# Optimization experiments

Measured on AMD Instinct MI355X. Metric: run time of the kernel, lower is better.

The kernel has to match this reference:

```python
import jax, jax.numpy as jnp
import numpy as np

B, L, DX, DQ = 8, 4096, 128, 128


def setup_inputs() -> dict:
    key = jax.random.key(0)
    ks = jax.random.split(key, 16)
    g = lambda k, shp, fan: jax.random.normal(k, shp, jnp.float32) * (1.0 / np.sqrt(fan))
    return {
        'x': jax.random.normal(ks[0], (B, L, DX), jnp.float32),
        'c': jax.random.normal(ks[1], (B, DQ), jnp.float32),
        # CrossAttention('add') params (all Linear weights stored as (in, out))
        'W1': g(ks[2], (DX, DX), DX),          # w1, bias frozen at 0
        'W2': g(ks[3], (DQ, DX), DQ),          # w2, bias frozen at 0
        'wt_w': g(ks[4], (DX,), DX),           # wt: dx -> 1, bias frozen at 0
        'bsa': jnp.zeros((DX,), jnp.float32),
        # csa pairwise-score params
        'Wsa1': g(ks[5], (DX, DX), DX),        # bias frozen at 0
        'Wsa2': g(ks[6], (DX, DX), DX),        # bias frozen at 0
        'wsat_w': g(ks[7], (DX,), DX),         # wsat: dx -> 1
        'wsat_b': jnp.zeros((), jnp.float32),
        'bsa1': jnp.zeros((DX,), jnp.float32),
        # PositionwiseFeedForward(dx, dx)
        'pfn_w1': g(ks[8], (DX, DX), DX),
        'pfn_b1': jnp.zeros((DX,), jnp.float32),
        'pfn_w2': g(ks[9], (DX, DX), DX),
        'pfn_b2': jnp.zeros((DX,), jnp.float32),
        'ln_g': jnp.ones((DX,), jnp.float32),
        'ln_b': jnp.zeros((DX,), jnp.float32),
    }


def reference(x, c, W1, W2, wt_w, bsa, Wsa1, Wsa2, wsat_w, wsat_b, bsa1,
              pfn_w1, pfn_b1, pfn_w2, pfn_b2, ln_g, ln_b):
    seq_len = x.shape[-2]
    # ---- CrossAttention, mode='add': p = softmax(wt(w1(x) + w2(c) + bsa), dim=-2) ----
    wx = jnp.einsum('bld,de->ble', x, W1)                 # (B, L, dx)
    wq = jnp.einsum('bd,de->be', c, W2)                   # (B, dx)
    logits = jnp.einsum('ble,e->bl', wx + wq[:, None, :] + bsa, wt_w)
    p = jax.nn.softmax(logits, axis=-1)[..., None]        # softmax over L -> (B, L, 1)
    h = x * p                                             # (B, L, dx)
    # ---- pairwise additive scores: wsat(Wsa1(h)_i + Wsa2(h)_j + bsa1) ----
    # wsat is linear, so the (B,L,L,dx) tensor decomposes exactly into rank-1 terms.
    si = jnp.einsum('ble,e->bl', jnp.einsum('bld,de->ble', h, Wsa1), wsat_w)  # (B, L)
    sj = jnp.einsum('ble,e->bl', jnp.einsum('bld,de->ble', h, Wsa2), wsat_w)  # (B, L)
    const = jnp.dot(bsa1, wsat_w) + wsat_b
    scores = jax.nn.sigmoid(si[:, :, None] + sj[:, None, :] + const)          # (B, L, L)
    # mask diagonal with -inf then softmax over last dim (j)
    diag = jnp.eye(seq_len, dtype=bool)
    scores = jnp.where(diag, -jnp.inf, scores)
    A = jax.nn.softmax(scores, axis=-1)                   # (B, L, L)
    # ui = sum_i A[b,i,j] * x[b,j,:]  (faithful to fcsa * x.unsqueeze(1) summed over dim 1)
    ui = x * jnp.sum(A, axis=1)[..., None]                # (B, L, dx)
    # ---- PositionwiseFeedForward with residual + LayerNorm(eps=1e-6); dropout=eval/identity ----
    y = jnp.maximum(jnp.einsum('bld,de->ble', ui, pfn_w1) + pfn_b1, 0.0)
    y = jnp.einsum('ble,ed->bld', y, pfn_w2) + pfn_b2 + ui
    mu = jnp.mean(y, axis=-1, keepdims=True)
    var = jnp.mean(jnp.square(y - mu), axis=-1, keepdims=True)
    return (y - mu) / jnp.sqrt(var + 1e-6) * ln_g + ln_b
```

## Files before the change

### kernel.cpp

```cpp
#include <hip/hip_runtime.h>


#define SEQ 4096
#define NB 8
#define DXC 128
#define SQRTE 1.6487212707001282f
#define Y1S 136

typedef __attribute__((ext_vector_type(8))) short short8;
typedef __attribute__((ext_vector_type(4))) float f32x4;

__device__ __forceinline__ float wave_sum(float v) {
#pragma unroll
  for (int m = 32; m >= 1; m >>= 1) v += __shfl_xor(v, m);
  return v;
}

__device__ __forceinline__ unsigned short f2bf(float f) {
  unsigned int u = __float_as_uint(f);
  unsigned int r = (u + 0x7FFFu + ((u >> 16) & 1u)) >> 16;
  return (unsigned short)r;
}

__device__ __forceinline__ void get_ck(float* ck) {
  ck[0] = 1.0f;
  ck[1] = 0.25f;
  ck[2] = 0.03125f;
  ck[3] = -7.0f / 384.0f;
  ck[4] = -31.0f / 6144.0f;
  ck[5] = 177.0f / 122880.0f;
  ck[6] = 2017.0f / 2949120.0f;
}

__device__ __forceinline__ float binomf(int k, int m) {
  const float B[7][7] = {
      {1, 0, 0, 0, 0, 0, 0},  {1, 1, 0, 0, 0, 0, 0},   {1, 2, 1, 0, 0, 0, 0},
      {1, 3, 3, 1, 0, 0, 0},  {1, 4, 6, 4, 1, 0, 0},   {1, 5, 10, 10, 5, 1, 0},
      {1, 6, 15, 20, 15, 6, 1}};
  return B[k][m];
}

__device__ __forceinline__ float g_exact(float t) {
  float sg = 1.0f / (1.0f + __expf(-t));
  return __expf(sg);
}

__global__ __launch_bounds__(256) void prep_pack(
    const float* __restrict__ W1, const float* __restrict__ W2,
    const float* __restrict__ Wsa1, const float* __restrict__ Wsa2,
    const float* __restrict__ wt_w, const float* __restrict__ wsat_w,
    const float* __restrict__ pw1, const float* __restrict__ pw2,
    float* __restrict__ vecs, unsigned short* __restrict__ Wt1,
    unsigned short* __restrict__ Wt2) {
  if (blockIdx.x < 128) {
    int wave = (blockIdx.x * 256 + threadIdx.x) >> 6;
    int lane = threadIdx.x & 63;
    int m = wave >> 7, d = wave & 127;
    const float* W = (m == 0) ? W1 : (m == 1) ? W2 : (m == 2) ? Wsa1 : Wsa2;
    const float* v = (m < 2) ? wt_w : wsat_w;
    float2 a = ((const float2*)(W + d * DXC))[lane];
    float2 b = ((const float2*)v)[lane];
    float s = wave_sum(a.x * b.x + a.y * b.y);
    if (lane == 0) vecs[m * DXC + d] = s;
  } else {
    int id = (blockIdx.x - 128) * 256 + threadIdx.x;
    int which = id >> 14;
    int k = id & 16383;
    int eo = k >> 7, d = k & 127;
    if (which == 0)
      Wt1[eo * DXC + d] = f2bf(pw1[d * DXC + eo]);
    else
      Wt2[eo * DXC + d] = f2bf(pw2[d * DXC + eo]);
  }
}

__global__ __launch_bounds__(256) void rowdots(
    const float* __restrict__ x, const float* __restrict__ vecs,
    float* __restrict__ t0, float* __restrict__ t1, float* __restrict__ t2) {
  int row = (blockIdx.x * 256 + threadIdx.x) >> 6;
  int lane = threadIdx.x & 63;
  float2 xv = ((const float2*)(x + (size_t)row * DXC))[lane];
  float2 a = ((const float2*)(vecs + 0))[lane];
  float2 b = ((const float2*)(vecs + 256))[lane];
  float2 d = ((const float2*)(vecs + 384))[lane];
  float s0 = wave_sum(xv.x * a.x + xv.y * a.y);
  float s1 = wave_sum(xv.x * b.x + xv.y * b.y);
  float s2 = wave_sum(xv.x * d.x + xv.y * d.y);
  if (lane == 0) { t0[row] = s0; t1[row] = s1; t2[row] = s2; }
}

__global__ __launch_bounds__(1024) void softmax_zq(
    const float* __restrict__ t0, const float* __restrict__ t1,
    const float* __restrict__ t2, const float* __restrict__ c,
    const float* __restrict__ bsa, const float* __restrict__ wt_w,
    const float* __restrict__ bsa1, const float* __restrict__ wsat_w,
    const float* __restrict__ wsat_b, const float* __restrict__ v2,
    float* __restrict__ sj, float* __restrict__ dcol,
    float* __restrict__ Qout) {
  __shared__ float red[16];
  __shared__ float red7[16][7];
  __shared__ float bc[4];
  __shared__ float Sv[8];
  __shared__ float Ps[7];
  int b = blockIdx.x, tid = threadIdx.x;
  if (tid < 64) {
    float2 cv = ((const float2*)(c + b * DXC))[tid];
    float2 vv = ((const float2*)v2)[tid];
    float2 ba = ((const float2*)bsa)[tid];
    float2 wt = ((const float2*)wt_w)[tid];
    float s = wave_sum(cv.x * vv.x + cv.y * vv.y + ba.x * wt.x + ba.y * wt.y);
    float2 b1 = ((const float2*)bsa1)[tid];
    float2 ww = ((const float2*)wsat_w)[tid];
    float t = wave_sum(b1.x * ww.x + b1.y * ww.y);
    if (tid == 0) { bc[2] = s; bc[3] = t + wsat_b[0]; }
  }
  float4 l4 = ((const float4*)(t0 + b * SEQ))[tid];
  __syncthreads();
  float cbv = bc[2], ccst = bc[3];
  l4.x += cbv; l4.y += cbv; l4.z += cbv; l4.w += cbv;
  float m = fmaxf(fmaxf(l4.x, l4.y), fmaxf(l4.z, l4.w));
#pragma unroll
  for (int s = 32; s >= 1; s >>= 1) m = fmaxf(m, __shfl_xor(m, s));
  if ((tid & 63) == 0) red[tid >> 6] = m;
  __syncthreads();
  if (tid < 16) {
    float v = red[tid];
#pragma unroll
    for (int s = 8; s >= 1; s >>= 1) v = fmaxf(v, __shfl_xor(v, s));
    if (tid == 0) bc[0] = v;
  }
  __syncthreads();
  float M = bc[0];
  float e0 = __expf(l4.x - M), e1 = __expf(l4.y - M);
  float e2 = __expf(l4.z - M), e3 = __expf(l4.w - M);
  float s = (e0 + e1) + (e2 + e3);
#pragma unroll
  for (int sh = 32; sh >= 1; sh >>= 1) s += __shfl_xor(s, sh);
  if ((tid & 63) == 0) red[tid >> 6] = s;
  __syncthreads();
  if (tid < 16) {
    float v = red[tid];
#pragma unroll
    for (int sh = 8; sh >= 1; sh >>= 1) v += __shfl_xor(v, sh);
    if (tid == 0) bc[1] = v;
  }
  __syncthreads();
  float inv = 1.0f / bc[1];
  float4 a4 = ((const float4*)(t1 + b * SEQ))[tid];
  float4 bb4 = ((const float4*)(t2 + b * SEQ))[tid];
  float av[4], bv[4];
  av[0] = e0 * inv * a4.x + ccst; av[1] = e1 * inv * a4.y + ccst;
  av[2] = e2 * inv * a4.z + ccst; av[3] = e3 * inv * a4.w + ccst;
  bv[0] = e0 * inv * bb4.x; bv[1] = e1 * inv * bb4.y;
  bv[2] = e2 * inv * bb4.z; bv[3] = e3 * inv * bb4.w;
  ((float4*)(sj + b * SEQ))[tid] = make_float4(bv[0], bv[1], bv[2], bv[3]);
  {
    float sm[6] = {0.f, 0.f, 0.f, 0.f, 0.f, 0.f};
#pragma unroll
    for (int e = 0; e < 4; ++e) {
      float t = bv[e];
#pragma unroll
      for (int n = 0; n < 6; ++n) { sm[n] += t; t *= bv[e]; }
    }
#pragma unroll
    for (int n = 0; n < 6; ++n) sm[n] = wave_sum(sm[n]);
    if ((tid & 63) == 0) {
#pragma unroll
      for (int n = 0; n < 6; ++n) red7[tid >> 6][n] = sm[n];
    }
  }
  __syncthreads();
  if (tid < 6) {
    float acc = 0.f;
#pragma unroll
    for (int w = 0; w < 16; ++w) acc += red7[w][tid];
    Sv[tid + 1] = acc;
  }
  if (tid == 6) Sv[0] = (float)SEQ;
  __syncthreads();
  if (tid < 7) {
    float ck[7];
    get_ck(ck);
    float acc = 0.f;
    for (int n = 0; n <= 6 - tid; ++n)
      acc += ck[tid + n] * binomf(tid + n, tid) * Sv[n];
    Ps[tid] = SQRTE * acc;
  }
  __syncthreads();
  float P0 = Ps[0], P1 = Ps[1], P2 = Ps[2], P3 = Ps[3], P4 = Ps[4],
        P5 = Ps[5], P6 = Ps[6];
  float acc[7] = {0.f, 0.f, 0.f, 0.f, 0.f, 0.f, 0.f};
  float4 dc;
  float* dcp = (float*)&dc;
#pragma unroll
  for (int e = 0; e < 4; ++e) {
    float a = av[e];
    float zf = ((((((P6 * a + P5) * a + P4) * a + P3) * a + P2) * a + P1) * a)
               + P0;
    float d = g_exact(a + bv[e]);
    float iz = 1.0f / (zf - d);
    dcp[e] = d * iz;
    float p = iz;
    acc[0] += p;
#pragma unroll
    for (int n = 1; n < 7; ++n) { p *= a; acc[n] += p; }
  }
  ((float4*)(dcol + b * SEQ))[tid] = dc;
#pragma unroll
  for (int n = 0; n < 7; ++n) acc[n] = wave_sum(acc[n]);
  if ((tid & 63) == 0) {
#pragma unroll
    for (int n = 0; n < 7; ++n) red7[tid >> 6][n] = acc[n];
  }
  __syncthreads();
  if (tid < 7) {
    float t = 0.f;
#pragma unroll
    for (int w = 0; w < 16; ++w) t += red7[w][tid];
    red[tid] = t;
  }
  __syncthreads();
  if (tid < 7) {
    float ck[7];
    get_ck(ck);
    float acc2 = 0.f;
    for (int n = 0; n <= 6 - tid; ++n)
      acc2 += ck[tid + n] * binomf(tid + n, tid) * red[n];
    Qout[b * 8 + tid] = SQRTE * acc2;
  }
}

__global__ __launch_bounds__(256) void ffn_mfma(
    const float* __restrict__ x, const float* __restrict__ sj,
    const float* __restrict__ dcol, const float* __restrict__ Q,
    const unsigned short* __restrict__ Wt1,
    const unsigned short* __restrict__ Wt2,
    const float* __restrict__ b1, const float* __restrict__ b2,
    const float* __restrict__ lng, const float* __restrict__ lnb,
    float* __restrict__ out) {
  __shared__ float cs[64];
  __shared__ __align__(16) unsigned short y1[64 * Y1S];
  int tid = threadIdx.x;
  int base = blockIdx.x * 64;
  int b = blockIdx.x >> 6;
  if (tid < 64) {
    int row = base + tid;
    float bb = sj[row];
    float q0 = Q[b * 8 + 0], q1 = Q[b * 8 + 1], q2 = Q[b * 8 + 2];
    float q3 = Q[b * 8 + 3], q4 = Q[b * 8 + 4], q5 = Q[b * 8 + 5];
    float q6 = Q[b * 8 + 6];
    cs[tid] = ((((((q6 * bb + q5) * bb + q4) * bb + q3) * bb + q2) * bb + q1)
              * bb + q0) - dcol[row];
  }
  __syncthreads();
  int lane = tid & 63, wave = tid >> 6;
  int n16 = lane & 15, quad = lane >> 4;
  int m0 = wave * 16;
  int rowA = base + m0 + n16;
  float csA = cs[m0 + n16];
  const float4* xr = (const float4*)(x + (size_t)rowA * DXC);
  short8 afr[4];
#pragma unroll
  for (int cc = 0; cc < 4; ++cc) {
    float4 p0 = xr[cc * 8 + quad * 2];
    float4 p1 = xr[cc * 8 + quad * 2 + 1];
    short8 af;
    af[0] = (short)f2bf(p0.x * csA); af[1] = (short)f2bf(p0.y * csA);
    af[2] = (short)f2bf(p0.z * csA); af[3] = (short)f2bf(p0.w * csA);
    af[4] = (short)f2bf(p1.x * csA); af[5] = (short)f2bf(p1.y * csA);
    af[6] = (short)f2bf(p1.z * csA); af[7] = (short)f2bf(p1.w * csA);
    afr[cc] = af;
  }
#pragma unroll
  for (int nt = 0; nt < 8; ++nt) {
    const unsigned short* wrow = Wt1 + (nt * 16 + n16) * DXC;
    f32x4 a = {0.f, 0.f, 0.f, 0.f};
#pragma unroll
    for (int cc = 0; cc < 4; ++cc) {
      short8 bf = *(const short8*)(wrow + cc * 32 + quad * 8);
      a = __builtin_amdgcn_mfma_f32_16x16x32_bf16(afr[cc], bf, a, 0, 0, 0);
    }
    float b1v = b1[nt * 16 + n16];
#pragma unroll
    for (int r = 0; r < 4; ++r) {
      float yv = fmaxf(a[r] + b1v, 0.f);
      y1[(m0 + quad * 4 + r) * Y1S + nt * 16 + n16] = f2bf(yv);
    }
  }
  __syncthreads();
  const unsigned short* yrow = &y1[(m0 + n16) * Y1S];
  short8 afr2[4];
#pragma unroll
  for (int cc = 0; cc < 4; ++cc)
    afr2[cc] = *(const short8*)(yrow + cc * 32 + quad * 8);
  f32x4 acc2[8];
#pragma unroll
  for (int nt = 0; nt < 8; ++nt) {
    const unsigned short* wrow = Wt2 + (nt * 16 + n16) * DXC;
    f32x4 a = {0.f, 0.f, 0.f, 0.f};
#pragma unroll
    for (int cc = 0; cc < 4; ++cc) {
      short8 bf = *(const short8*)(wrow + cc * 32 + quad * 8);
      a = __builtin_amdgcn_mfma_f32_16x16x32_bf16(afr2[cc], bf, a, 0, 0, 0);
    }
    acc2[nt] = a;
  }
  float b2v[8], lgv[8], lbv[8];
#pragma unroll
  for (int nt = 0; nt < 8; ++nt) {
    int col = nt * 16 + n16;
    b2v[nt] = b2[col]; lgv[nt] = lng[col]; lbv[nt] = lnb[col];
  }
#pragma unroll
  for (int r = 0; r < 4; ++r) {
    int rl = m0 + quad * 4 + r;
    int row = base + rl;
    float csr = cs[rl];
    const float* xrow = x + (size_t)row * DXC;
    float z[8];
    float s = 0.f, sq = 0.f;
#pragma unroll
    for (int nt = 0; nt < 8; ++nt) {
      int col = nt * 16 + n16;
      float zz = acc2[nt][r] + b2v[nt] + xrow[col] * csr;
      z[nt] = zz; s += zz; sq += zz * zz;
    }
#pragma unroll
    for (int mm = 8; mm >= 1; mm >>= 1) {
      s += __shfl_xor(s, mm);
      sq += __shfl_xor(sq, mm);
    }
    float mu = s * 0.0078125f;
    float var = sq * 0.0078125f - mu * mu;
    float rstd = 1.0f / sqrtf(var + 1e-6f);
    float* orow = out + (size_t)row * DXC;
#pragma unroll
    for (int nt = 0; nt < 8; ++nt) {
      int col = nt * 16 + n16;
      orow[col] = (z[nt] - mu) * rstd * lgv[nt] + lbv[nt];
    }
  }
}

extern "C" void kernel_launch(void* const* d_in, const int* in_sizes, int n_in,
                              void* d_out, int out_size, void* d_ws, size_t ws_size,
                              hipStream_t stream) {
  const float* x = (const float*)d_in[0];
  const float* cc = (const float*)d_in[1];
  const float* W1 = (const float*)d_in[2];
  const float* W2 = (const float*)d_in[3];
  const float* wt_w = (const float*)d_in[4];
  const float* bsa = (const float*)d_in[5];
  const float* Wsa1 = (const float*)d_in[6];
  const float* Wsa2 = (const float*)d_in[7];
  const float* wsat_w = (const float*)d_in[8];
  const float* wsat_b = (const float*)d_in[9];
  const float* bsa1 = (const float*)d_in[10];
  const float* pw1 = (const float*)d_in[11];
  const float* pb1 = (const float*)d_in[12];
  const float* pw2 = (const float*)d_in[13];
  const float* pb2 = (const float*)d_in[14];
  const float* lng = (const float*)d_in[15];
  const float* lnb = (const float*)d_in[16];
  float* out = (float*)d_out;
  float* ws = (float*)d_ws;

  const int NR = NB * SEQ;
  float* vecs = ws;
  float* Q = ws + 512;
  float* t0 = ws + 1024;
  float* t1 = t0 + NR;
  float* t2 = t1 + NR;
  float* sj = t2 + NR;
  float* dcol = sj + NR;
  unsigned short* Wt1 = (unsigned short*)(ws + 164864);
  unsigned short* Wt2 = (unsigned short*)(ws + 164864 + 8192);

  prep_pack<<<256, 256, 0, stream>>>(W1, W2, Wsa1, Wsa2, wt_w, wsat_w, pw1,
                                     pw2, vecs, Wt1, Wt2);
  rowdots<<<NR / 4, 256, 0, stream>>>(x, vecs, t0, t1, t2);
  softmax_zq<<<NB, 1024, 0, stream>>>(t0, t1, t2, cc, bsa, wt_w, bsa1, wsat_w,
                                      wsat_b, vecs + 128, sj, dcol, Q);
  ffn_mfma<<<NR / 64, 256, 0, stream>>>(x, sj, dcol, Q, Wt1, Wt2, pb1, pb2,
                                        lng, lnb, out);
}
```

Measured before the change: 137.4 us.

## Fuse weight prep, row dots and softmax into one per-batch front kernel

Merges prep_pack, rowdots and softmax_zq into a single kernel with one 1024-thread block per batch. Each block computes the weight-vector projections into shared memory, streams its batch's 4096 rows of x to compute the three row dots into shared memory, then runs the softmax and moment reductions. It also drops the softmax max-subtraction and the c/bsa logit offset, since a constant shift cancels in the softmax. This removes two launches and the global round trips for t0/t1/t2, but the 16 MB read of x now runs on only 8 workgroups, which risks being far slower than the wide rowdots grid.

```diff
diff --git a/kernel.cpp b/kernel.cpp
--- a/kernel.cpp
+++ b/kernel.cpp
@@ -13,6 +13,12 @@
 __device__ __forceinline__ float wave_sum(float v) {
 #pragma unroll
   for (int m = 32; m >= 1; m >>= 1) v += __shfl_xor(v, m);
+  return v;
+}
+
+__device__ __forceinline__ float qwave_sum(float v) {
+#pragma unroll
+  for (int m = 8; m >= 1; m >>= 1) v += __shfl_xor(v, m);
   return v;
 }
 
@@ -45,179 +51,173 @@
   return __expf(sg);
 }
 
-__global__ __launch_bounds__(256) void prep_pack(
-    const float* __restrict__ W1, const float* __restrict__ W2,
+__global__ __launch_bounds__(1024) void fused_front(
+    const float* __restrict__ x, const float* __restrict__ W1,
     const float* __restrict__ Wsa1, const float* __restrict__ Wsa2,
     const float* __restrict__ wt_w, const float* __restrict__ wsat_w,
+    const float* __restrict__ wsat_b, const float* __restrict__ bsa1,
     const float* __restrict__ pw1, const float* __restrict__ pw2,
-    float* __restrict__ vecs, unsigned short* __restrict__ Wt1,
-    unsigned short* __restrict__ Wt2) {
-  if (blockIdx.x < 128) {
-    int wave = (blockIdx.x * 256 + threadIdx.x) >> 6;
-    int lane = threadIdx.x & 63;
-    int m = wave >> 7, d = wave & 127;
-    const float* W = (m == 0) ? W1 : (m == 1) ? W2 : (m == 2) ? Wsa1 : Wsa2;
-    const float* v = (m < 2) ? wt_w : wsat_w;
-    float2 a = ((const float2*)(W + d * DXC))[lane];
-    float2 b = ((const float2*)v)[lane];
-    float s = wave_sum(a.x * b.x + a.y * b.y);
-    if (lane == 0) vecs[m * DXC + d] = s;
-  } else {
-    int id = (blockIdx.x - 128) * 256 + threadIdx.x;
-    int which = id >> 14;
-    int k = id & 16383;
-    int eo = k >> 7, d = k & 127;
-    if (which == 0)
-      Wt1[eo * DXC + d] = f2bf(pw1[d * DXC + eo]);
-    else
-      Wt2[eo * DXC + d] = f2bf(pw2[d * DXC + eo]);
-  }
-}
-
-__global__ __launch_bounds__(256) void rowdots(
-    const float* __restrict__ x, const float* __restrict__ vecs,
-    float* __restrict__ t0, float* __restrict__ t1, float* __restrict__ t2) {
-  int row = (blockIdx.x * 256 + threadIdx.x) >> 6;
-  int lane = threadIdx.x & 63;
-  float2 xv = ((const float2*)(x + (size_t)row * DXC))[lane];
-  float2 a = ((const float2*)(vecs + 0))[lane];
-  float2 b = ((const float2*)(vecs + 256))[lane];
-  float2 d = ((const float2*)(vecs + 384))[lane];
-  float s0 = wave_sum(xv.x * a.x + xv.y * a.y);
-  float s1 = wave_sum(xv.x * b.x + xv.y * b.y);
-  float s2 = wave_sum(xv.x * d.x + xv.y * d.y);
-  if (lane == 0) { t0[row] = s0; t1[row] = s1; t2[row] = s2; }
-}
-
-__global__ __launch_bounds__(1024) void softmax_zq(
-    const float* __restrict__ t0, const float* __restrict__ t1,
-    const float* __restrict__ t2, const float* __restrict__ c,
-    const float* __restrict__ bsa, const float* __restrict__ wt_w,
-    const float* __restrict__ bsa1, const float* __restrict__ wsat_w,
-    const float* __restrict__ wsat_b, const float* __restrict__ v2,
+    unsigned short* __restrict__ Wt1, unsigned short* __restrict__ Wt2,
     float* __restrict__ sj, float* __restrict__ dcol,
     float* __restrict__ Qout) {
-  __shared__ float red[16];
-  __shared__ float red7[16][7];
-  __shared__ float bc[4];
-  __shared__ float Sv[8];
-  __shared__ float Ps[7];
+  __shared__ float vs[3 * DXC];
+  __shared__ __align__(16) float t0s[SEQ];
+  __shared__ __align__(16) float t1s[SEQ];
+  __shared__ __align__(16) float t2s[SEQ];
+  __shared__ float red[16][8];
+  __shared__ float bcast[8];
+  __shared__ float Ps[8];
+  __shared__ float ccst_s;
+
   int b = blockIdx.x, tid = threadIdx.x;
-  if (tid < 64) {
-    float2 cv = ((const float2*)(c + b * DXC))[tid];
-    float2 vv = ((const float2*)v2)[tid];
-    float2 ba = ((const float2*)bsa)[tid];
-    float2 wt = ((const float2*)wt_w)[tid];
-    float s = wave_sum(cv.x * vv.x + cv.y * vv.y + ba.x * wt.x + ba.y * wt.y);
-    float2 b1 = ((const float2*)bsa1)[tid];
-    float2 ww = ((const float2*)wsat_w)[tid];
-    float t = wave_sum(b1.x * ww.x + b1.y * ww.y);
-    if (tid == 0) { bc[2] = s; bc[3] = t + wsat_b[0]; }
-  }
-  float4 l4 = ((const float4*)(t0 + b * SEQ))[tid];
-  __syncthreads();
-  float cbv = bc[2], ccst = bc[3];
-  l4.x += cbv; l4.y += cbv; l4.z += cbv; l4.w += cbv;
-  float m = fmaxf(fmaxf(l4.x, l4.y), fmaxf(l4.z, l4.w));
-#pragma unroll
-  for (int s = 32; s >= 1; s >>= 1) m = fmaxf(m, __shfl_xor(m, s));
-  if ((tid & 63) == 0) red[tid >> 6] = m;
-  __syncthreads();
-  if (tid < 16) {
-    float v = red[tid];
-#pragma unroll
-    for (int s = 8; s >= 1; s >>= 1) v = fmaxf(v, __shfl_xor(v, s));
-    if (tid == 0) bc[0] = v;
-  }
-  __syncthreads();
-  float M = bc[0];
-  float e0 = __expf(l4.x - M), e1 = __expf(l4.y - M);
-  float e2 = __expf(l4.z - M), e3 = __expf(l4.w - M);
-  float s = (e0 + e1) + (e2 + e3);
-#pragma unroll
-  for (int sh = 32; sh >= 1; sh >>= 1) s += __shfl_xor(s, sh);
-  if ((tid & 63) == 0) red[tid >> 6] = s;
-  __syncthreads();
-  if (tid < 16) {
-    float v = red[tid];
-#pragma unroll
-    for (int sh = 8; sh >= 1; sh >>= 1) v += __shfl_xor(v, sh);
-    if (tid == 0) bc[1] = v;
-  }
-  __syncthreads();
-  float inv = 1.0f / bc[1];
-  float4 a4 = ((const float4*)(t1 + b * SEQ))[tid];
-  float4 bb4 = ((const float4*)(t2 + b * SEQ))[tid];
+  if (tid < 384) {
+    int m = tid >> 7, d = tid & 127;
+    const float* W = (m == 0) ? W1 : (m == 1) ? Wsa1 : Wsa2;
+    const float* v = (m == 0) ? wt_w : wsat_w;
+    const float4* Wr = (const float4*)(W + d * DXC);
+    const float4* vr = (const float4*)v;
+    float acc = 0.f;
+#pragma unroll 4
+    for (int e = 0; e < 32; ++e) {
+      float4 w4 = Wr[e]; float4 v4 = vr[e];
+      acc += w4.x * v4.x + w4.y * v4.y + w4.z * v4.z + w4.w * v4.w;
+    }
+    vs[m * DXC + d] = acc;
+  } else if (tid == 384) {
+    const float4* Wr = (const float4*)bsa1;
+    const float4* vr = (const float4*)wsat_w;
+    float acc = 0.f;
+    for (int e = 0; e < 32; ++e) {
+      float4 w4 = Wr[e]; float4 v4 = vr[e];
+      acc += w4.x * v4.x + w4.y * v4.y + w4.z * v4.z + w4.w * v4.w;
+    }
+    ccst_s = acc + wsat_b[0];
+  } else if (tid >= 512) {
+    int t = tid - 512;
+    int which = t >> 8;
+    int eo = b * 16 + ((t >> 4) & 15);
+    int d0 = (t & 15) * 8;
+    const float* pw = which ? pw2 : pw1;
+    unsigned short* Wt = which ? Wt2 : Wt1;
+#pragma unroll
+    for (int k = 0; k < 8; ++k)
+      Wt[eo * DXC + d0 + k] = f2bf(pw[(d0 + k) * DXC + eo]);
+  }
+  __syncthreads();
+
+  int lane = tid & 63, wave = tid >> 6;
+  int seg = lane & 15, sub = lane >> 4;
+  float4 v00 = *(const float4*)&vs[0 * DXC + seg * 8];
+  float4 v01 = *(const float4*)&vs[0 * DXC + seg * 8 + 4];
+  float4 v10 = *(const float4*)&vs[1 * DXC + seg * 8];
+  float4 v11 = *(const float4*)&vs[1 * DXC + seg * 8 + 4];
+  float4 v20 = *(const float4*)&vs[2 * DXC + seg * 8];
+  float4 v21 = *(const float4*)&vs[2 * DXC + seg * 8 + 4];
+  const float* xb = x + (size_t)b * SEQ * DXC;
+#pragma unroll 4
+  for (int p = 0; p < 64; ++p) {
+    int r = p * 64 + wave * 4 + sub;
+    const float4* xp = (const float4*)(xb + (size_t)r * DXC + seg * 8);
+    float4 lo = xp[0], hi = xp[1];
+    float s0 = lo.x * v00.x + lo.y * v00.y + lo.z * v00.z + lo.w * v00.w
+             + hi.x * v01.x + hi.y * v01.y + hi.z * v01.z + hi.w * v01.w;
+    float s1 = lo.x * v10.x + lo.y * v10.y + lo.z * v10.z + lo.w * v10.w
+             + hi.x * v11.x + hi.y * v11.y + hi.z * v11.z + hi.w * v11.w;
+    float s2 = lo.x * v20.x + lo.y * v20.y + lo.z * v20.z + lo.w * v20.w
+             + hi.x * v21.x + hi.y * v21.y + hi.z * v21.z + hi.w * v21.w;
+    s0 = qwave_sum(s0);
+    s1 = qwave_sum(s1);
+    s2 = qwave_sum(s2);
+    if (seg == 0) { t0s[r] = s0; t1s[r] = s1; t2s[r] = s2; }
+  }
+  __syncthreads();
+
+  float e4[4], t1r[4], t2r[4];
+  float ssum = 0.f;
+#pragma unroll
+  for (int k = 0; k < 4; ++k) {
+    int r = k * 1024 + tid;
+    e4[k] = __expf(t0s[r]);
+    t1r[k] = t1s[r];
+    t2r[k] = t2s[r];
+    ssum += e4[k];
+  }
+  ssum = wave_sum(ssum);
+  if (lane == 0) red[wave][0] = ssum;
+  __syncthreads();
+  if (tid == 0) {
+    float t = 0.f;
+    for (int w = 0; w < 16; ++w) t += red[w][0];
+    Ps[7] = 1.0f / t;
+  }
+  __syncthreads();
+  float invS = Ps[7];
+  float ccst = ccst_s;
   float av[4], bv[4];
-  av[0] = e0 * inv * a4.x + ccst; av[1] = e1 * inv * a4.y + ccst;
-  av[2] = e2 * inv * a4.z + ccst; av[3] = e3 * inv * a4.w + ccst;
-  bv[0] = e0 * inv * bb4.x; bv[1] = e1 * inv * bb4.y;
-  bv[2] = e2 * inv * bb4.z; bv[3] = e3 * inv * bb4.w;
-  ((float4*)(sj + b * SEQ))[tid] = make_float4(bv[0], bv[1], bv[2], bv[3]);
-  {
-    float sm[6] = {0.f, 0.f, 0.f, 0.f, 0.f, 0.f};
-#pragma unroll
-    for (int e = 0; e < 4; ++e) {
-      float t = bv[e];
-#pragma unroll
-      for (int n = 0; n < 6; ++n) { sm[n] += t; t *= bv[e]; }
-    }
-#pragma unroll
-    for (int n = 0; n < 6; ++n) sm[n] = wave_sum(sm[n]);
-    if ((tid & 63) == 0) {
-#pragma unroll
-      for (int n = 0; n < 6; ++n) red7[tid >> 6][n] = sm[n];
-    }
+#pragma unroll
+  for (int k = 0; k < 4; ++k) {
+    float p = e4[k] * invS;
+    av[k] = p * t1r[k] + ccst;
+    bv[k] = p * t2r[k];
+    sj[b * SEQ + k * 1024 + tid] = bv[k];
+  }
+  float sm[6] = {0.f, 0.f, 0.f, 0.f, 0.f, 0.f};
+#pragma unroll
+  for (int k = 0; k < 4; ++k) {
+    float t = bv[k];
+#pragma unroll
+    for (int n = 0; n < 6; ++n) { sm[n] += t; t *= bv[k]; }
+  }
+#pragma unroll
+  for (int n = 0; n < 6; ++n) sm[n] = wave_sum(sm[n]);
+  if (lane == 0) {
+#pragma unroll
+    for (int n = 0; n < 6; ++n) red[wave][n] = sm[n];
   }
   __syncthreads();
   if (tid < 6) {
     float acc = 0.f;
-#pragma unroll
-    for (int w = 0; w < 16; ++w) acc += red7[w][tid];
-    Sv[tid + 1] = acc;
-  }
-  if (tid == 6) Sv[0] = (float)SEQ;
+    for (int w = 0; w < 16; ++w) acc += red[w][tid];
+    bcast[tid + 1] = acc;
+  }
+  if (tid == 6) bcast[0] = (float)SEQ;
   __syncthreads();
   if (tid < 7) {
     float ck[7];
     get_ck(ck);
     float acc = 0.f;
     for (int n = 0; n <= 6 - tid; ++n)
-      acc += ck[tid + n] * binomf(tid + n, tid) * Sv[n];
+      acc += ck[tid + n] * binomf(tid + n, tid) * bcast[n];
     Ps[tid] = SQRTE * acc;
   }
   __syncthreads();
   float P0 = Ps[0], P1 = Ps[1], P2 = Ps[2], P3 = Ps[3], P4 = Ps[4],
         P5 = Ps[5], P6 = Ps[6];
-  float acc[7] = {0.f, 0.f, 0.f, 0.f, 0.f, 0.f, 0.f};
-  float4 dc;
-  float* dcp = (float*)&dc;
-#pragma unroll
-  for (int e = 0; e < 4; ++e) {
-    float a = av[e];
+  float acc7[7] = {0.f, 0.f, 0.f, 0.f, 0.f, 0.f, 0.f};
+#pragma unroll
+  for (int k = 0; k < 4; ++k) {
+    float a = av[k];
     float zf = ((((((P6 * a + P5) * a + P4) * a + P3) * a + P2) * a + P1) * a)
                + P0;
-    float d = g_exact(a + bv[e]);
+    float d = g_exact(a + bv[k]);
     float iz = 1.0f / (zf - d);
-    dcp[e] = d * iz;
+    dcol[b * SEQ + k * 1024 + tid] = d * iz;
     float p = iz;
-    acc[0] += p;
-#pragma unroll
-    for (int n = 1; n < 7; ++n) { p *= a; acc[n] += p; }
-  }
-  ((float4*)(dcol + b * SEQ))[tid] = dc;
-#pragma unroll
-  for (int n = 0; n < 7; ++n) acc[n] = wave_sum(acc[n]);
-  if ((tid & 63) == 0) {
-#pragma unroll
-    for (int n = 0; n < 7; ++n) red7[tid >> 6][n] = acc[n];
+    acc7[0] += p;
+#pragma unroll
+    for (int n = 1; n < 7; ++n) { p *= a; acc7[n] += p; }
+  }
+#pragma unroll
+  for (int n = 0; n < 7; ++n) acc7[n] = wave_sum(acc7[n]);
+  if (lane == 0) {
+#pragma unroll
+    for (int n = 0; n < 7; ++n) red[wave][n] = acc7[n];
   }
   __syncthreads();
   if (tid < 7) {
     float t = 0.f;
-#pragma unroll
-    for (int w = 0; w < 16; ++w) t += red7[w][tid];
-    red[tid] = t;
+    for (int w = 0; w < 16; ++w) t += red[w][tid];
+    bcast[tid] = t;
   }
   __syncthreads();
   if (tid < 7) {
@@ -225,7 +225,7 @@
     get_ck(ck);
     float acc2 = 0.f;
     for (int n = 0; n <= 6 - tid; ++n)
-      acc2 += ck[tid + n] * binomf(tid + n, tid) * red[n];
+      acc2 += ck[tid + n] * binomf(tid + n, tid) * bcast[n];
     Qout[b * 8 + tid] = SQRTE * acc2;
   }
 }
@@ -346,11 +346,8 @@
                               void* d_out, int out_size, void* d_ws, size_t ws_size,
                               hipStream_t stream) {
   const float* x = (const float*)d_in[0];
-  const float* cc = (const float*)d_in[1];
   const float* W1 = (const float*)d_in[2];
-  const float* W2 = (const float*)d_in[3];
   const float* wt_w = (const float*)d_in[4];
-  const float* bsa = (const float*)d_in[5];
   const float* Wsa1 = (const float*)d_in[6];
   const float* Wsa2 = (const float*)d_in[7];
   const float* wsat_w = (const float*)d_in[8];
@@ -366,21 +363,15 @@
   float* ws = (float*)d_ws;
 
   const int NR = NB * SEQ;
-  float* vecs = ws;
-  float* Q = ws + 512;
-  float* t0 = ws + 1024;
-  float* t1 = t0 + NR;
-  float* t2 = t1 + NR;
-  float* sj = t2 + NR;
-  float* dcol = sj + NR;
-  unsigned short* Wt1 = (unsigned short*)(ws + 164864);
-  unsigned short* Wt2 = (unsigned short*)(ws + 164864 + 8192);
-
-  prep_pack<<<256, 256, 0, stream>>>(W1, W2, Wsa1, Wsa2, wt_w, wsat_w, pw1,
-                                     pw2, vecs, Wt1, Wt2);
-  rowdots<<<NR / 4, 256, 0, stream>>>(x, vecs, t0, t1, t2);
-  softmax_zq<<<NB, 1024, 0, stream>>>(t0, t1, t2, cc, bsa, wt_w, bsa1, wsat_w,
-                                      wsat_b, vecs + 128, sj, dcol, Q);
-  ffn_mfma<<<NR / 64, 256, 0, stream>>>(x, sj, dcol, Q, Wt1, Wt2, pb1, pb2,
+  float* Q = ws;
+  float* sjW = ws + 512;
+  float* dcolW = sjW + NR;
+  unsigned short* Wt1 = (unsigned short*)(dcolW + NR);
+  unsigned short* Wt2 = Wt1 + DXC * DXC;
+
+  fused_front<<<NB, 1024, 0, stream>>>(x, W1, Wsa1, Wsa2, wt_w, wsat_w,
+                                       wsat_b, bsa1, pw1, pw2, Wt1, Wt2, sjW,
+                                       dcolW, Q);
+  ffn_mfma<<<NR / 64, 256, 0, stream>>>(x, sjW, dcolW, Q, Wt1, Wt2, pb1, pb2,
                                         lng, lnb, out);
 }
```

New measurement: 174.6 us. +27.1%, slower.
